# Performance work log

Hardware: AMD Instinct MI355X
Metric: run time of the kernel (lower is better)

## Reference

```python
import jax, jax.numpy as jnp
import numpy as np

N_GROUPS = 32
EPS = 1e-5
N_HEADS = 4
D_K = 64


def group_norm(x, gamma, beta):
    # x: [B, C, H, W]; normalize over (channels within group, spatial)
    B, C, H, W = x.shape
    xg = x.reshape(B, N_GROUPS, C // N_GROUPS, H, W)
    mean = jnp.mean(xg, axis=(2, 3, 4), keepdims=True)
    var = jnp.var(xg, axis=(2, 3, 4), keepdims=True)
    xn = ((xg - mean) * jax.lax.rsqrt(var + EPS)).reshape(B, C, H, W)
    return xn * gamma[None, :, None, None] + beta[None, :, None, None]


def setup_inputs() -> dict:
    key = jax.random.key(0)
    ks = jax.random.split(key, 4)
    B, C, H, W = 4, 256, 64, 64
    x = jax.random.normal(ks[0], (B, C, H, W), dtype=jnp.float32)
    gamma = jnp.ones((C,), dtype=jnp.float32)
    beta = jnp.zeros((C,), dtype=jnp.float32)
    w_qkv = jax.random.normal(ks[1], (C, N_HEADS * D_K * 3), dtype=jnp.float32) * (C ** -0.5)
    b_qkv = jnp.zeros((N_HEADS * D_K * 3,), dtype=jnp.float32)
    w_out = jax.random.normal(ks[2], (N_HEADS * D_K, C), dtype=jnp.float32) * ((N_HEADS * D_K) ** -0.5)
    b_out = jnp.zeros((C,), dtype=jnp.float32)
    return {"x": x, "gamma": gamma, "beta": beta, "w_qkv": w_qkv,
            "b_qkv": b_qkv, "w_out": w_out, "b_out": b_out}


def reference(x, gamma, beta, w_qkv, b_qkv, w_out, b_out):
    B, C, H, W = x.shape
    S = H * W
    scale = D_K ** -0.5
    # GroupNorm -> [B, S, C]
    h = group_norm(x, gamma, beta).reshape(B, C, S).transpose(0, 2, 1)
    qkv = (h @ w_qkv + b_qkv).reshape(B, S, N_HEADS, 3 * D_K)
    q, k, v = jnp.split(qkv, 3, axis=-1)          # each [B, S, H, D]
    attn = jnp.einsum('bihd,bjhd->bijh', q, k) * scale
    attn = jax.nn.softmax(attn, axis=2)           # softmax over j (keys)
    res = jnp.einsum('bijh,bjhd->bihd', attn, v)  # [B, S, H, D]
    res = res.reshape(B, S, N_HEADS * D_K)
    res = res @ w_out + b_out                     # [B, S, C]
    res = res.transpose(0, 2, 1).reshape(B, C, H, W)
    return res + x
```

## Files before the change

kernel.cpp:

```cpp
#include <hip/hip_runtime.h>
#include <hip/hip_bf16.h>


typedef __attribute__((ext_vector_type(8))) short short8;
typedef __attribute__((ext_vector_type(4))) float f32x4;
typedef __attribute__((ext_vector_type(16))) float f32x16;

__device__ __forceinline__ unsigned short f2bf(float f) {
    union { float f; unsigned u; } v; v.f = f;
    unsigned r = v.u + 0x7FFF + ((v.u >> 16) & 1);
    return (unsigned short)(r >> 16);
}

__device__ __forceinline__ unsigned cvt_pk_bf16(float lo, float hi) {
    unsigned r;
    asm("v_cvt_pk_bf16_f32 %0, %1, %2" : "=v"(r) : "v"(lo), "v"(hi));
    return r;
}

__device__ __forceinline__ void permswap(unsigned &x, unsigned &y) {
    asm("v_permlane32_swap_b32 %0, %1" : "+v"(x), "+v"(y));
}

__device__ __forceinline__ float fexp2(float x) {
    float r;
    asm("v_exp_f32 %0, %1" : "=v"(r) : "v"(x));
    return r;
}

__device__ __forceinline__ void gl_lds16(const void* g, void* l) {
    __builtin_amdgcn_global_load_lds(
        (const __attribute__((address_space(1))) void*)(g),
        (__attribute__((address_space(3))) void*)(l), 16, 0, 0);
}

__device__ __forceinline__ f32x16 fzero16() {
    f32x16 z;
    #pragma unroll
    for (int i = 0; i < 16; ++i) z[i] = 0.f;
    return z;
}

__global__ __launch_bounds__(1024) void k_pre(
    const float* __restrict__ x, float* __restrict__ stats,
    const float* __restrict__ wqkv, const float* __restrict__ wout,
    unsigned short* __restrict__ wqkvT, unsigned short* __restrict__ woutT) {
    if (blockIdx.x < 128) {
        int bg = blockIdx.x;
        const float4* xp = (const float4*)(x + bg * 32768);
        float s1 = 0.f, s2 = 0.f;
        for (int i = threadIdx.x; i < 8192; i += 1024) {
            float4 v = xp[i];
            s1 += v.x + v.y + v.z + v.w;
            s2 += v.x*v.x + v.y*v.y + v.z*v.z + v.w*v.w;
        }
        #pragma unroll
        for (int off = 32; off; off >>= 1) {
            s1 += __shfl_down(s1, off);
            s2 += __shfl_down(s2, off);
        }
        __shared__ float r1[16], r2[16];
        int wid = threadIdx.x >> 6;
        if ((threadIdx.x & 63) == 0) { r1[wid] = s1; r2[wid] = s2; }
        __syncthreads();
        if (threadIdx.x == 0) {
            float a = 0.f, b = 0.f;
            #pragma unroll
            for (int i = 0; i < 16; ++i) { a += r1[i]; b += r2[i]; }
            float mean = a * (1.f/32768.f);
            float var  = b * (1.f/32768.f) - mean*mean;
            stats[bg*2]   = mean;
            stats[bg*2+1] = rsqrtf(var + 1e-5f);
        }
    } else {
        int i = (blockIdx.x - 128) * 1024 + threadIdx.x;
        if (i < 196608) {
            int k = i / 768, n = i - k * 768;
            wqkvT[n*256 + k] = f2bf(wqkv[i]);
        }
        if (i < 65536) {
            int k = i >> 8, n = i & 255;
            woutT[n*256 + k] = f2bf(wout[i]);
        }
    }
}

__global__ __launch_bounds__(512, 2) void k_qkvf(
    const float* __restrict__ x, const float* __restrict__ gamma,
    const float* __restrict__ beta, const float* __restrict__ stats,
    const unsigned short* __restrict__ wT, const float* __restrict__ bqkv,
    unsigned short* __restrict__ q, unsigned short* __restrict__ kk,
    unsigned short* __restrict__ vT) {
    __shared__ unsigned short t[64][72];
    __shared__ unsigned short lds_h[64][272];

    int m0 = blockIdx.x * 64;
    int b = m0 >> 12;
    int s0 = m0 & 4095;
    int tid = threadIdx.x;

    #pragma unroll
    for (int cb = 0; cb < 4; ++cb) {
        int c0 = cb * 64;
        #pragma unroll
        for (int k = 0; k < 2; ++k) {
            int u = tid + k * 512;
            int cr = u >> 4;
            int sl = (u & 15) * 4;
            int c = c0 + cr;
            float4 v = *(const float4*)&x[(b*256 + c)*4096 + s0 + sl];
            int sg = (b*32 + (c >> 3)) * 2;
            float mean = stats[sg], rstd = stats[sg+1];
            float sa = rstd * gamma[c];
            float sb = beta[c] - mean * sa;
            ushort4 pk;
            pk.x = f2bf(v.x*sa + sb); pk.y = f2bf(v.y*sa + sb);
            pk.z = f2bf(v.z*sa + sb); pk.w = f2bf(v.w*sa + sb);
            *(ushort4*)&t[cr][sl] = pk;
        }
        __syncthreads();
        int sr = tid >> 3;
        int cc8 = (tid & 7) * 8;
        unsigned rr[4];
        #pragma unroll
        for (int j = 0; j < 4; ++j)
            rr[j] = (unsigned)t[cc8 + 2*j][sr] | ((unsigned)t[cc8 + 2*j + 1][sr] << 16);
        *(uint4*)&lds_h[sr][c0 + cc8] = make_uint4(rr[0], rr[1], rr[2], rr[3]);
        __syncthreads();
    }

    int wid = tid >> 6, lane = tid & 63;
    int g = lane >> 4, li = lane & 15;
    int rg = wid & 1, cg = wid >> 1;
    f32x4 acc[2][12];
    #pragma unroll
    for (int rt = 0; rt < 2; ++rt)
        #pragma unroll
        for (int nt = 0; nt < 12; ++nt) acc[rt][nt] = (f32x4){0.f,0.f,0.f,0.f};
    #pragma unroll
    for (int kt = 0; kt < 8; ++kt) {
        short8 a0 = *(const short8*)&lds_h[rg*32 + li][kt*32 + g*8];
        short8 a1 = *(const short8*)&lds_h[rg*32 + 16 + li][kt*32 + g*8];
        #pragma unroll
        for (int nt = 0; nt < 12; ++nt) {
            int n = cg*192 + nt*16 + li;
            short8 bb = *(const short8*)&wT[n*256 + kt*32 + g*8];
            acc[0][nt] = __builtin_amdgcn_mfma_f32_16x16x32_bf16(a0, bb, acc[0][nt], 0, 0, 0);
            acc[1][nt] = __builtin_amdgcn_mfma_f32_16x16x32_bf16(a1, bb, acc[1][nt], 0, 0, 0);
        }
    }
    int bh = b*4 + cg;
    #pragma unroll
    for (int rt = 0; rt < 2; ++rt) {
        int s0w = s0 + rg*32 + rt*16;
        #pragma unroll
        for (int nt = 0; nt < 12; ++nt) {
            int ng = cg*192 + nt*16 + li;
            float bias = bqkv[ng];
            int d = (nt & 3)*16 + li;
            if ((nt >> 2) == 2) {
                ushort4 pk;
                pk.x = f2bf(acc[rt][nt][0] + bias); pk.y = f2bf(acc[rt][nt][1] + bias);
                pk.z = f2bf(acc[rt][nt][2] + bias); pk.w = f2bf(acc[rt][nt][3] + bias);
                *(ushort4*)&vT[(bh*64 + d)*4096 + s0w + g*4] = pk;
            } else if ((nt >> 2) == 0) {
                #pragma unroll
                for (int r = 0; r < 4; ++r)
                    q[(bh*4096 + s0w + g*4 + r)*64 + d] = f2bf((acc[rt][nt][r] + bias) * 0.1803368801f);
            } else {
                #pragma unroll
                for (int r = 0; r < 4; ++r)
                    kk[(bh*4096 + s0w + g*4 + r)*64 + d] = f2bf(acc[rt][nt][r] + bias);
            }
        }
    }
}

__global__ __launch_bounds__(512, 4) void k_attn(
    const unsigned short* __restrict__ q, const unsigned short* __restrict__ kk,
    const unsigned short* __restrict__ vT, unsigned short* __restrict__ ao) {
    __shared__ __align__(16) char smem[65536];

    int n = blockIdx.x;
    int qt = n >> 4;
    int bh = ((n & 7) << 1) | ((n >> 3) & 1);
    int tid = threadIdx.x;
    int wid = tid >> 6, lane = tid & 63;
    int qw = wid & 3, st = wid >> 2;
    int hi = lane >> 5, il = lane & 31;
    int swl = (il & 7) << 4;

    int qbase = qt * 128 + qw * 32;
    int qrow = bh * 4096 + qbase + il;
    short8 bq[4];
    #pragma unroll
    for (int kc = 0; kc < 4; ++kc)
        bq[kc] = *(const short8*)&q[qrow*64 + kc*16 + hi*8];

    short8 ones;
    #pragma unroll
    for (int i = 0; i < 8; ++i) ones[i] = (short)0x3F80;

    unsigned p16  = tid * 16;
    unsigned row0 = p16 >> 7;
    unsigned sw   = (row0 & 7) << 4;
    unsigned ks0  = p16 ^ sw;
    unsigned vc0  = (p16 & 127u) ^ sw;
    const char* kbase = (const char*)kk + (size_t)bh * 524288;
    const char* vbase = (const char*)vT + (size_t)(bh*64 + row0) * 8192;
    unsigned woff = wid * 1024;

#define STAGE_PAIR(d, pair) do {                                             \
    const char* _k0 = kbase + (size_t)(2*(pair)) * 8192;                     \
    size_t _vo = (size_t)(2*(pair)) * 128;                                   \
    gl_lds16(_k0 + ks0,              smem + ((d)*2+0)*8192 + woff);          \
    gl_lds16(_k0 + 8192 + ks0,       smem + ((d)*2+1)*8192 + woff);          \
    gl_lds16(vbase + _vo + vc0,       smem + 32768 + ((d)*2+0)*8192 + woff); \
    gl_lds16(vbase + _vo + 128 + vc0, smem + 32768 + ((d)*2+1)*8192 + woff); \
} while (0)

    f32x16 o0 = fzero16(), o1 = fzero16(), accl = fzero16();
    float m_run = 0.f;

    STAGE_PAIR(0, 0);
    asm volatile("s_waitcnt vmcnt(0)" ::: "memory");
    __builtin_amdgcn_s_barrier();
    asm volatile("" ::: "memory");

    int cur = 0;
    for (int tp = 0; tp < 32; ++tp) {
        if (tp < 31) STAGE_PAIR(cur ^ 1, tp + 1);

        const char* kb = smem + (cur*2 + st) * 8192;
        const char* vb = smem + 32768 + (cur*2 + st) * 8192;

        float nm = -m_run;
        f32x16 p0, p1;
        #pragma unroll
        for (int r = 0; r < 16; ++r) { p0[r] = nm; p1[r] = nm; }
        __builtin_amdgcn_s_setprio(1);
        #pragma unroll
        for (int kc = 0; kc < 4; ++kc) {
            int c = (kc*32 + hi*16) ^ swl;
            short8 ka0 = *(const short8*)(kb + il*128 + c);
            short8 ka1 = *(const short8*)(kb + 4096 + il*128 + c);
            p0 = __builtin_amdgcn_mfma_f32_32x32x16_bf16(ka0, bq[kc], p0, 0, 0, 0);
            p1 = __builtin_amdgcn_mfma_f32_32x32x16_bf16(ka1, bq[kc], p1, 0, 0, 0);
        }
        __builtin_amdgcn_s_setprio(0);

        #pragma unroll
        for (int r = 0; r < 16; ++r) {
            p0[r] = fexp2(p0[r]);
            p1[r] = fexp2(p1[r]);
        }
        float m8[8];
        #pragma unroll
        for (int r = 0; r < 8; ++r)
            m8[r] = fmaxf(fmaxf(p0[2*r], p0[2*r+1]), fmaxf(p1[2*r], p1[2*r+1]));
        float pm = fmaxf(fmaxf(fmaxf(m8[0], m8[1]), fmaxf(m8[2], m8[3])),
                         fmaxf(fmaxf(m8[4], m8[5]), fmaxf(m8[6], m8[7])));
        if (__any(pm > 16.f)) {
            pm = fmaxf(pm, __shfl_xor(pm, 32));
            float fac = 1.f / pm;
            m_run += log2f(pm);
            accl[0] *= fac;
            #pragma unroll
            for (int r = 0; r < 16; ++r) {
                o0[r] *= fac; o1[r] *= fac;
                p0[r] *= fac; p1[r] *= fac;
            }
        }

        __builtin_amdgcn_s_setprio(1);
        #pragma unroll
        for (int jc = 0; jc < 4; ++jc) {
            const int hh = jc & 1;
            float e0, e1, e2, e3, e4, e5, e6, e7;
            if (jc < 2) {
                e0 = p0[hh*8+0]; e1 = p0[hh*8+1]; e2 = p0[hh*8+2]; e3 = p0[hh*8+3];
                e4 = p0[hh*8+4]; e5 = p0[hh*8+5]; e6 = p0[hh*8+6]; e7 = p0[hh*8+7];
            } else {
                e0 = p1[hh*8+0]; e1 = p1[hh*8+1]; e2 = p1[hh*8+2]; e3 = p1[hh*8+3];
                e4 = p1[hh*8+4]; e5 = p1[hh*8+5]; e6 = p1[hh*8+6]; e7 = p1[hh*8+7];
            }
            unsigned a = cvt_pk_bf16(e0, e1);
            unsigned b = cvt_pk_bf16(e2, e3);
            unsigned c = cvt_pk_bf16(e4, e5);
            unsigned d = cvt_pk_bf16(e6, e7);
            permswap(a, c);
            permswap(b, d);
            union { unsigned u[4]; short8 s8; } pb;
            pb.u[0] = a; pb.u[1] = b; pb.u[2] = c; pb.u[3] = d;
            int co = (jc*32 + hi*16) ^ swl;
            short8 va0 = *(const short8*)(vb + il*128 + co);
            short8 va1 = *(const short8*)(vb + 4096 + il*128 + co);
            o0   = __builtin_amdgcn_mfma_f32_32x32x16_bf16(va0, pb.s8, o0, 0, 0, 0);
            o1   = __builtin_amdgcn_mfma_f32_32x32x16_bf16(va1, pb.s8, o1, 0, 0, 0);
            accl = __builtin_amdgcn_mfma_f32_32x32x16_bf16(ones, pb.s8, accl, 0, 0, 0);
        }
        __builtin_amdgcn_s_setprio(0);

        if (tp < 31) asm volatile("s_waitcnt vmcnt(0)" ::: "memory");
        asm volatile("" ::: "memory");
        __builtin_amdgcn_s_barrier();
        asm volatile("" ::: "memory");
        cur ^= 1;
    }
#undef STAGE_PAIR

    float l_loc = accl[0];

    float* red = (float*)smem;
    int slot = ((qw*64 + lane) * 34);
    if (st == 1) {
        #pragma unroll
        for (int r = 0; r < 16; ++r) { red[slot + r] = o0[r]; red[slot + 16 + r] = o1[r]; }
        red[slot + 32] = l_loc;
        red[slot + 33] = m_run;
    }
    __syncthreads();
    if (st == 0) {
        float m1 = red[slot + 33], l1 = red[slot + 32];
        float m = fmaxf(m_run, m1);
        float f0 = fexp2(m_run - m), f1 = fexp2(m1 - m);
        float inv = 1.f / (l_loc * f0 + l1 * f1);
        float a0 = f0 * inv, a1 = f1 * inv;
        int b = bh >> 2, hh = bh & 3;
        int s = qbase + il;
        unsigned short* aop = &ao[((size_t)(b*4096 + s))*256 + hh*64];
        #pragma unroll
        for (int rr = 0; rr < 4; ++rr) {
            ushort4 pk0, pk1;
            pk0.x = f2bf(o0[rr*4+0]*a0 + red[slot + rr*4+0]*a1);
            pk0.y = f2bf(o0[rr*4+1]*a0 + red[slot + rr*4+1]*a1);
            pk0.z = f2bf(o0[rr*4+2]*a0 + red[slot + rr*4+2]*a1);
            pk0.w = f2bf(o0[rr*4+3]*a0 + red[slot + rr*4+3]*a1);
            *(ushort4*)&aop[rr*8 + hi*4] = pk0;
            pk1.x = f2bf(o1[rr*4+0]*a0 + red[slot + 16 + rr*4+0]*a1);
            pk1.y = f2bf(o1[rr*4+1]*a0 + red[slot + 16 + rr*4+1]*a1);
            pk1.z = f2bf(o1[rr*4+2]*a0 + red[slot + 16 + rr*4+2]*a1);
            pk1.w = f2bf(o1[rr*4+3]*a0 + red[slot + 16 + rr*4+3]*a1);
            *(ushort4*)&aop[32 + rr*8 + hi*4] = pk1;
        }
    }
}

__global__ __launch_bounds__(512) void k_out(
    const unsigned short* __restrict__ ao, const unsigned short* __restrict__ wT,
    const float* __restrict__ bout, const float* __restrict__ x,
    float* __restrict__ out) {
    __shared__ float lds_fT[256][68];
    int mt = blockIdx.x;
    int tid = threadIdx.x;
    int wid = tid >> 6, lane = tid & 63;
    int g = lane >> 4, li = lane & 15;
    int rg = wid & 3, ch = wid >> 2;
    int m0 = mt * 64;
    int row = m0 + rg*16 + li;
    f32x4 acc[8];
    #pragma unroll
    for (int nt = 0; nt < 8; ++nt) acc[nt] = (f32x4){0.f,0.f,0.f,0.f};
    #pragma unroll
    for (int kt = 0; kt < 8; ++kt) {
        short8 a = *(const short8*)&ao[row*256 + kt*32 + g*8];
        #pragma unroll
        for (int nt = 0; nt < 8; ++nt) {
            int nn = ch*128 + nt*16 + li;
            short8 b = *(const short8*)&wT[nn*256 + kt*32 + g*8];
            acc[nt] = __builtin_amdgcn_mfma_f32_16x16x32_bf16(a, b, acc[nt], 0, 0, 0);
        }
    }
    #pragma unroll
    for (int nt = 0; nt < 8; ++nt) {
        int c = ch*128 + nt*16 + li;
        float bias = bout[c];
        #pragma unroll
        for (int r = 0; r < 4; ++r)
            lds_fT[c][rg*16 + g*4 + r] = acc[nt][r] + bias;
    }
    __syncthreads();
    int b = m0 >> 12;
    int s0 = m0 & 4095;
    #pragma unroll
    for (int p = 0; p < 8; ++p) {
        int c = p*32 + (tid >> 4);
        int sl = (tid & 15) * 4;
        float4 t = *(const float4*)&lds_fT[c][sl];
        int base = (b*256 + c)*4096 + s0 + sl;
        float4 xr = *(const float4*)&x[base];
        t.x += xr.x; t.y += xr.y; t.z += xr.z; t.w += xr.w;
        *(float4*)&out[base] = t;
    }
}

extern "C" void kernel_launch(void* const* d_in, const int* in_sizes, int n_in,
                              void* d_out, int out_size, void* d_ws, size_t ws_size,
                              hipStream_t stream) {
    (void)in_sizes; (void)n_in; (void)out_size; (void)ws_size;
    const float* x     = (const float*)d_in[0];
    const float* gamma = (const float*)d_in[1];
    const float* beta  = (const float*)d_in[2];
    const float* wqkv  = (const float*)d_in[3];
    const float* bqkv  = (const float*)d_in[4];
    const float* wout  = (const float*)d_in[5];
    const float* bout  = (const float*)d_in[6];
    float* out = (float*)d_out;

    char* ws = (char*)d_ws;
    unsigned short* q     = (unsigned short*)(ws + (8u<<20));
    unsigned short* kk    = (unsigned short*)(ws + (16u<<20));
    unsigned short* vT    = (unsigned short*)(ws + (24u<<20));
    unsigned short* ao    = (unsigned short*)(ws + (32u<<20));
    unsigned short* wqkvT = (unsigned short*)(ws + (40u<<20));
    unsigned short* woutT = (unsigned short*)(ws + (40u<<20) + 393216);
    float*          stats = (float*)(ws + (40u<<20) + 524288);

    k_pre<<<320, 1024, 0, stream>>>(x, stats, wqkv, wout, wqkvT, woutT);
    k_qkvf<<<256, 512, 0, stream>>>(x, gamma, beta, stats, wqkvT, bqkv, q, kk, vT);
    k_attn<<<dim3(512), 512, 0, stream>>>(q, kk, vT, ao);
    k_out<<<dim3(256), 512, 0, stream>>>(ao, woutT, bout, x, out);
}
```

Measured before the change: 150.6 us.

## Give each attention wave two query tiles and compute row sums with VALU

The attention kernel drops from 8 to 4 waves per block. Each wave now handles 64 queries as two 32-row tiles, so every K and V fragment read from LDS feeds two MFMAs, which halves LDS read traffic per FLOP. The row-sum MFMA against a ones vector is replaced by VALU adds plus a cross-half shuffle. Each thread now issues twice as many global-to-LDS loads and holds many more live accumulators, which raises register pressure and reduces wave-level parallelism.

```diff
diff --git a/kernel.cpp b/kernel.cpp
--- a/kernel.cpp
+++ b/kernel.cpp
@@ -176,7 +176,7 @@
     }
 }
 
-__global__ __launch_bounds__(512, 4) void k_attn(
+__global__ __launch_bounds__(256, 2) void k_attn(
     const unsigned short* __restrict__ q, const unsigned short* __restrict__ kk,
     const unsigned short* __restrict__ vT, unsigned short* __restrict__ ao) {
     __shared__ __align__(16) char smem[65536];
@@ -186,118 +186,152 @@
     int bh = ((n & 7) << 1) | ((n >> 3) & 1);
     int tid = threadIdx.x;
     int wid = tid >> 6, lane = tid & 63;
-    int qw = wid & 3, st = wid >> 2;
+    int qw = wid & 1, st = wid >> 1;
     int hi = lane >> 5, il = lane & 31;
     int swl = (il & 7) << 4;
 
-    int qbase = qt * 128 + qw * 32;
-    int qrow = bh * 4096 + qbase + il;
-    short8 bq[4];
-    #pragma unroll
-    for (int kc = 0; kc < 4; ++kc)
-        bq[kc] = *(const short8*)&q[qrow*64 + kc*16 + hi*8];
-
-    short8 ones;
-    #pragma unroll
-    for (int i = 0; i < 8; ++i) ones[i] = (short)0x3F80;
+    int qbase = qt * 128 + qw * 64;
+    short8 bqA[4], bqB[4];
+    #pragma unroll
+    for (int kc = 0; kc < 4; ++kc) {
+        bqA[kc] = *(const short8*)&q[(bh*4096 + qbase + il)*64 + kc*16 + hi*8];
+        bqB[kc] = *(const short8*)&q[(bh*4096 + qbase + 32 + il)*64 + kc*16 + hi*8];
+    }
 
     unsigned p16  = tid * 16;
     unsigned row0 = p16 >> 7;
     unsigned sw   = (row0 & 7) << 4;
     unsigned ks0  = p16 ^ sw;
     unsigned vc0  = (p16 & 127u) ^ sw;
-    const char* kbase = (const char*)kk + (size_t)bh * 524288;
-    const char* vbase = (const char*)vT + (size_t)(bh*64 + row0) * 8192;
+    const char* kbase  = (const char*)kk + (size_t)bh * 524288;
+    const char* vbase0 = (const char*)vT + (size_t)(bh*64 + row0) * 8192;
+    const char* vbase1 = vbase0 + (size_t)32 * 8192;
     unsigned woff = wid * 1024;
 
-#define STAGE_PAIR(d, pair) do {                                             \
-    const char* _k0 = kbase + (size_t)(2*(pair)) * 8192;                     \
-    size_t _vo = (size_t)(2*(pair)) * 128;                                   \
-    gl_lds16(_k0 + ks0,              smem + ((d)*2+0)*8192 + woff);          \
-    gl_lds16(_k0 + 8192 + ks0,       smem + ((d)*2+1)*8192 + woff);          \
-    gl_lds16(vbase + _vo + vc0,       smem + 32768 + ((d)*2+0)*8192 + woff); \
-    gl_lds16(vbase + _vo + 128 + vc0, smem + 32768 + ((d)*2+1)*8192 + woff); \
+#define STAGE(d, pair) do {                                                   \
+    const char* _k0 = kbase + (size_t)(2*(pair)) * 8192;                      \
+    const char* _k1 = _k0 + 8192;                                             \
+    size_t _v0 = (size_t)(2*(pair)) * 128;                                    \
+    size_t _v1 = _v0 + 128;                                                   \
+    char* kd0 = smem + ((d)*2+0)*8192 + woff;                                 \
+    char* kd1 = smem + ((d)*2+1)*8192 + woff;                                 \
+    char* vd0 = smem + 32768 + ((d)*2+0)*8192 + woff;                         \
+    char* vd1 = smem + 32768 + ((d)*2+1)*8192 + woff;                         \
+    gl_lds16(_k0 + ks0,            kd0);                                      \
+    gl_lds16(_k0 + 4096 + ks0,     kd0 + 4096);                               \
+    gl_lds16(_k1 + ks0,            kd1);                                      \
+    gl_lds16(_k1 + 4096 + ks0,     kd1 + 4096);                               \
+    gl_lds16(vbase0 + _v0 + vc0,   vd0);                                      \
+    gl_lds16(vbase1 + _v0 + vc0,   vd0 + 4096);                               \
+    gl_lds16(vbase0 + _v1 + vc0,   vd1);                                      \
+    gl_lds16(vbase1 + _v1 + vc0,   vd1 + 4096);                               \
 } while (0)
 
-    f32x16 o0 = fzero16(), o1 = fzero16(), accl = fzero16();
-    float m_run = 0.f;
-
-    STAGE_PAIR(0, 0);
+    f32x16 oA0 = fzero16(), oA1 = fzero16();
+    f32x16 oB0 = fzero16(), oB1 = fzero16();
+    float lA = 0.f, lB = 0.f, m_run = 0.f;
+
+    STAGE(0, 0);
     asm volatile("s_waitcnt vmcnt(0)" ::: "memory");
     __builtin_amdgcn_s_barrier();
     asm volatile("" ::: "memory");
 
     int cur = 0;
     for (int tp = 0; tp < 32; ++tp) {
-        if (tp < 31) STAGE_PAIR(cur ^ 1, tp + 1);
+        if (tp < 31) STAGE(cur ^ 1, tp + 1);
 
         const char* kb = smem + (cur*2 + st) * 8192;
         const char* vb = smem + 32768 + (cur*2 + st) * 8192;
 
         float nm = -m_run;
-        f32x16 p0, p1;
-        #pragma unroll
-        for (int r = 0; r < 16; ++r) { p0[r] = nm; p1[r] = nm; }
+        f32x16 pA0, pA1, pB0, pB1;
+        #pragma unroll
+        for (int r = 0; r < 16; ++r) { pA0[r] = nm; pA1[r] = nm; pB0[r] = nm; pB1[r] = nm; }
         __builtin_amdgcn_s_setprio(1);
         #pragma unroll
         for (int kc = 0; kc < 4; ++kc) {
             int c = (kc*32 + hi*16) ^ swl;
             short8 ka0 = *(const short8*)(kb + il*128 + c);
             short8 ka1 = *(const short8*)(kb + 4096 + il*128 + c);
-            p0 = __builtin_amdgcn_mfma_f32_32x32x16_bf16(ka0, bq[kc], p0, 0, 0, 0);
-            p1 = __builtin_amdgcn_mfma_f32_32x32x16_bf16(ka1, bq[kc], p1, 0, 0, 0);
+            pA0 = __builtin_amdgcn_mfma_f32_32x32x16_bf16(ka0, bqA[kc], pA0, 0, 0, 0);
+            pB0 = __builtin_amdgcn_mfma_f32_32x32x16_bf16(ka0, bqB[kc], pB0, 0, 0, 0);
+            pA1 = __builtin_amdgcn_mfma_f32_32x32x16_bf16(ka1, bqA[kc], pA1, 0, 0, 0);
+            pB1 = __builtin_amdgcn_mfma_f32_32x32x16_bf16(ka1, bqB[kc], pB1, 0, 0, 0);
         }
         __builtin_amdgcn_s_setprio(0);
 
         #pragma unroll
         for (int r = 0; r < 16; ++r) {
-            p0[r] = fexp2(p0[r]);
-            p1[r] = fexp2(p1[r]);
-        }
-        float m8[8];
-        #pragma unroll
-        for (int r = 0; r < 8; ++r)
-            m8[r] = fmaxf(fmaxf(p0[2*r], p0[2*r+1]), fmaxf(p1[2*r], p1[2*r+1]));
-        float pm = fmaxf(fmaxf(fmaxf(m8[0], m8[1]), fmaxf(m8[2], m8[3])),
-                         fmaxf(fmaxf(m8[4], m8[5]), fmaxf(m8[6], m8[7])));
+            pA0[r] = fexp2(pA0[r]); pA1[r] = fexp2(pA1[r]);
+            pB0[r] = fexp2(pB0[r]); pB1[r] = fexp2(pB1[r]);
+        }
+        float mm[8];
+        #pragma unroll
+        for (int r = 0; r < 8; ++r) {
+            float a = fmaxf(fmaxf(pA0[2*r], pA0[2*r+1]), fmaxf(pA1[2*r], pA1[2*r+1]));
+            float b = fmaxf(fmaxf(pB0[2*r], pB0[2*r+1]), fmaxf(pB1[2*r], pB1[2*r+1]));
+            mm[r] = fmaxf(a, b);
+        }
+        float pm = fmaxf(fmaxf(fmaxf(mm[0], mm[1]), fmaxf(mm[2], mm[3])),
+                         fmaxf(fmaxf(mm[4], mm[5]), fmaxf(mm[6], mm[7])));
         if (__any(pm > 16.f)) {
             pm = fmaxf(pm, __shfl_xor(pm, 32));
             float fac = 1.f / pm;
             m_run += log2f(pm);
-            accl[0] *= fac;
+            lA *= fac; lB *= fac;
             #pragma unroll
             for (int r = 0; r < 16; ++r) {
-                o0[r] *= fac; o1[r] *= fac;
-                p0[r] *= fac; p1[r] *= fac;
+                oA0[r] *= fac; oA1[r] *= fac; oB0[r] *= fac; oB1[r] *= fac;
+                pA0[r] *= fac; pA1[r] *= fac; pB0[r] *= fac; pB1[r] *= fac;
             }
+        }
+        {
+            float a8[8], b8[8];
+            #pragma unroll
+            for (int r = 0; r < 8; ++r) {
+                a8[r] = (pA0[2*r] + pA0[2*r+1]) + (pA1[2*r] + pA1[2*r+1]);
+                b8[r] = (pB0[2*r] + pB0[2*r+1]) + (pB1[2*r] + pB1[2*r+1]);
+            }
+            float psA = ((a8[0]+a8[1]) + (a8[2]+a8[3])) + ((a8[4]+a8[5]) + (a8[6]+a8[7]));
+            float psB = ((b8[0]+b8[1]) + (b8[2]+b8[3])) + ((b8[4]+b8[5]) + (b8[6]+b8[7]));
+            psA += __shfl_xor(psA, 32);
+            psB += __shfl_xor(psB, 32);
+            lA += psA; lB += psB;
         }
 
         __builtin_amdgcn_s_setprio(1);
         #pragma unroll
         for (int jc = 0; jc < 4; ++jc) {
             const int hh = jc & 1;
-            float e0, e1, e2, e3, e4, e5, e6, e7;
+            float eA0, eA1, eA2, eA3, eA4, eA5, eA6, eA7;
+            float eB0, eB1, eB2, eB3, eB4, eB5, eB6, eB7;
             if (jc < 2) {
-                e0 = p0[hh*8+0]; e1 = p0[hh*8+1]; e2 = p0[hh*8+2]; e3 = p0[hh*8+3];
-                e4 = p0[hh*8+4]; e5 = p0[hh*8+5]; e6 = p0[hh*8+6]; e7 = p0[hh*8+7];
+                eA0=pA0[hh*8+0]; eA1=pA0[hh*8+1]; eA2=pA0[hh*8+2]; eA3=pA0[hh*8+3];
+                eA4=pA0[hh*8+4]; eA5=pA0[hh*8+5]; eA6=pA0[hh*8+6]; eA7=pA0[hh*8+7];
+                eB0=pB0[hh*8+0]; eB1=pB0[hh*8+1]; eB2=pB0[hh*8+2]; eB3=pB0[hh*8+3];
+                eB4=pB0[hh*8+4]; eB5=pB0[hh*8+5]; eB6=pB0[hh*8+6]; eB7=pB0[hh*8+7];
             } else {
-                e0 = p1[hh*8+0]; e1 = p1[hh*8+1]; e2 = p1[hh*8+2]; e3 = p1[hh*8+3];
-                e4 = p1[hh*8+4]; e5 = p1[hh*8+5]; e6 = p1[hh*8+6]; e7 = p1[hh*8+7];
+                eA0=pA1[hh*8+0]; eA1=pA1[hh*8+1]; eA2=pA1[hh*8+2]; eA3=pA1[hh*8+3];
+                eA4=pA1[hh*8+4]; eA5=pA1[hh*8+5]; eA6=pA1[hh*8+6]; eA7=pA1[hh*8+7];
+                eB0=pB1[hh*8+0]; eB1=pB1[hh*8+1]; eB2=pB1[hh*8+2]; eB3=pB1[hh*8+3];
+                eB4=pB1[hh*8+4]; eB5=pB1[hh*8+5]; eB6=pB1[hh*8+6]; eB7=pB1[hh*8+7];
             }
-            unsigned a = cvt_pk_bf16(e0, e1);
-            unsigned b = cvt_pk_bf16(e2, e3);
-            unsigned c = cvt_pk_bf16(e4, e5);
-            unsigned d = cvt_pk_bf16(e6, e7);
-            permswap(a, c);
-            permswap(b, d);
-            union { unsigned u[4]; short8 s8; } pb;
-            pb.u[0] = a; pb.u[1] = b; pb.u[2] = c; pb.u[3] = d;
+            unsigned a0 = cvt_pk_bf16(eA0, eA1), b0 = cvt_pk_bf16(eA2, eA3);
+            unsigned c0 = cvt_pk_bf16(eA4, eA5), d0 = cvt_pk_bf16(eA6, eA7);
+            permswap(a0, c0); permswap(b0, d0);
+            unsigned a1 = cvt_pk_bf16(eB0, eB1), b1 = cvt_pk_bf16(eB2, eB3);
+            unsigned c1 = cvt_pk_bf16(eB4, eB5), d1 = cvt_pk_bf16(eB6, eB7);
+            permswap(a1, c1); permswap(b1, d1);
+            union { unsigned u[4]; short8 s8; } pbA, pbB;
+            pbA.u[0]=a0; pbA.u[1]=b0; pbA.u[2]=c0; pbA.u[3]=d0;
+            pbB.u[0]=a1; pbB.u[1]=b1; pbB.u[2]=c1; pbB.u[3]=d1;
             int co = (jc*32 + hi*16) ^ swl;
             short8 va0 = *(const short8*)(vb + il*128 + co);
             short8 va1 = *(const short8*)(vb + 4096 + il*128 + co);
-            o0   = __builtin_amdgcn_mfma_f32_32x32x16_bf16(va0, pb.s8, o0, 0, 0, 0);
-            o1   = __builtin_amdgcn_mfma_f32_32x32x16_bf16(va1, pb.s8, o1, 0, 0, 0);
-            accl = __builtin_amdgcn_mfma_f32_32x32x16_bf16(ones, pb.s8, accl, 0, 0, 0);
+            oA0 = __builtin_amdgcn_mfma_f32_32x32x16_bf16(va0, pbA.s8, oA0, 0, 0, 0);
+            oB0 = __builtin_amdgcn_mfma_f32_32x32x16_bf16(va0, pbB.s8, oB0, 0, 0, 0);
+            oA1 = __builtin_amdgcn_mfma_f32_32x32x16_bf16(va1, pbA.s8, oA1, 0, 0, 0);
+            oB1 = __builtin_amdgcn_mfma_f32_32x32x16_bf16(va1, pbB.s8, oB1, 0, 0, 0);
         }
         __builtin_amdgcn_s_setprio(0);
 
@@ -307,41 +341,48 @@
         asm volatile("" ::: "memory");
         cur ^= 1;
     }
-#undef STAGE_PAIR
-
-    float l_loc = accl[0];
+#undef STAGE
 
     float* red = (float*)smem;
-    int slot = ((qw*64 + lane) * 34);
+    int b = bh >> 2, hh = bh & 3;
     if (st == 1) {
-        #pragma unroll
-        for (int r = 0; r < 16; ++r) { red[slot + r] = o0[r]; red[slot + 16 + r] = o1[r]; }
-        red[slot + 32] = l_loc;
-        red[slot + 33] = m_run;
+        int s0 = ((qw*2 + 0)*64 + lane) * 34;
+        int s1 = ((qw*2 + 1)*64 + lane) * 34;
+        #pragma unroll
+        for (int r = 0; r < 16; ++r) {
+            red[s0 + r] = oA0[r]; red[s0 + 16 + r] = oA1[r];
+            red[s1 + r] = oB0[r]; red[s1 + 16 + r] = oB1[r];
+        }
+        red[s0 + 32] = lA; red[s0 + 33] = m_run;
+        red[s1 + 32] = lB; red[s1 + 33] = m_run;
     }
     __syncthreads();
     if (st == 0) {
-        float m1 = red[slot + 33], l1 = red[slot + 32];
-        float m = fmaxf(m_run, m1);
-        float f0 = fexp2(m_run - m), f1 = fexp2(m1 - m);
-        float inv = 1.f / (l_loc * f0 + l1 * f1);
-        float a0 = f0 * inv, a1 = f1 * inv;
-        int b = bh >> 2, hh = bh & 3;
-        int s = qbase + il;
-        unsigned short* aop = &ao[((size_t)(b*4096 + s))*256 + hh*64];
-        #pragma unroll
-        for (int rr = 0; rr < 4; ++rr) {
-            ushort4 pk0, pk1;
-            pk0.x = f2bf(o0[rr*4+0]*a0 + red[slot + rr*4+0]*a1);
-            pk0.y = f2bf(o0[rr*4+1]*a0 + red[slot + rr*4+1]*a1);
-            pk0.z = f2bf(o0[rr*4+2]*a0 + red[slot + rr*4+2]*a1);
-            pk0.w = f2bf(o0[rr*4+3]*a0 + red[slot + rr*4+3]*a1);
-            *(ushort4*)&aop[rr*8 + hi*4] = pk0;
-            pk1.x = f2bf(o1[rr*4+0]*a0 + red[slot + 16 + rr*4+0]*a1);
-            pk1.y = f2bf(o1[rr*4+1]*a0 + red[slot + 16 + rr*4+1]*a1);
-            pk1.z = f2bf(o1[rr*4+2]*a0 + red[slot + 16 + rr*4+2]*a1);
-            pk1.w = f2bf(o1[rr*4+3]*a0 + red[slot + 16 + rr*4+3]*a1);
-            *(ushort4*)&aop[32 + rr*8 + hi*4] = pk1;
+        #pragma unroll
+        for (int qb = 0; qb < 2; ++qb) {
+            int slot = ((qw*2 + qb)*64 + lane) * 34;
+            float myl = qb ? lB : lA;
+            float m1 = red[slot + 33], l1 = red[slot + 32];
+            float m = fmaxf(m_run, m1);
+            float f0 = fexp2(m_run - m), f1 = fexp2(m1 - m);
+            float inv = 1.f / (myl * f0 + l1 * f1);
+            float a0 = f0 * inv, a1 = f1 * inv;
+            int s = qbase + qb*32 + il;
+            unsigned short* aop = &ao[((size_t)(b*4096 + s))*256 + hh*64];
+            #pragma unroll
+            for (int rr = 0; rr < 4; ++rr) {
+                float o0v[4], o1v[4];
+                #pragma unroll
+                for (int r = 0; r < 4; ++r) {
+                    o0v[r] = (qb ? oB0[rr*4+r] : oA0[rr*4+r]) * a0 + red[slot + rr*4+r] * a1;
+                    o1v[r] = (qb ? oB1[rr*4+r] : oA1[rr*4+r]) * a0 + red[slot + 16 + rr*4+r] * a1;
+                }
+                ushort4 pk0, pk1;
+                pk0.x = f2bf(o0v[0]); pk0.y = f2bf(o0v[1]); pk0.z = f2bf(o0v[2]); pk0.w = f2bf(o0v[3]);
+                pk1.x = f2bf(o1v[0]); pk1.y = f2bf(o1v[1]); pk1.z = f2bf(o1v[2]); pk1.w = f2bf(o1v[3]);
+                *(ushort4*)&aop[rr*8 + hi*4] = pk0;
+                *(ushort4*)&aop[32 + rr*8 + hi*4] = pk1;
+            }
         }
     }
 }
@@ -418,6 +459,6 @@
 
     k_pre<<<320, 1024, 0, stream>>>(x, stats, wqkv, wout, wqkvT, woutT);
     k_qkvf<<<256, 512, 0, stream>>>(x, gamma, beta, stats, wqkvT, bqkv, q, kk, vT);
-    k_attn<<<dim3(512), 512, 0, stream>>>(q, kk, vT, ao);
+    k_attn<<<dim3(512), 256, 0, stream>>>(q, kk, vT, ao);
     k_out<<<dim3(256), 512, 0, stream>>>(ao, woutT, bout, x, out);
 }
```

New measurement: 269.6 us. 1.79x slower.
